# Optimization experiments

Measured on AMD Instinct MI355X. Metric: run time of the kernel, lower is better.

## Reference

```python
import jax, jax.numpy as jnp
import numpy as np
import math

B, D = 4096, 2048  # batch, input_size == hidden_size


def setup_inputs() -> dict:
    key = jax.random.key(0)
    ks = jax.random.split(key, 9)
    stdv = 1.0 / math.sqrt(D)
    u = lambda k, shp: jax.random.uniform(k, shp, jnp.float32, -stdv, stdv)
    return {
        "inputs": jax.random.normal(ks[0], (B, D), jnp.float32),
        "frac_n": jax.random.normal(ks[1], (B, D), jnp.float32),
        "frac_d": jax.random.uniform(ks[2], (B, D), jnp.float32, 0.1, 1.0),
        "scale": jax.random.normal(ks[3], (B, D), jnp.float32),
        "w_r": u(ks[4], (D, D)),
        "w_k": u(ks[5], (D, D)),
        "w_v": u(ks[6], (D, D)),
        "w_o": u(ks[7], (D, D)),
        "w_u": jnp.ones((D,), jnp.float32),  # init.ones_ for 1-D params
        "w_w": jnp.ones((D,), jnp.float32),
    }


def reference(inputs, frac_n, frac_d, scale, w_r, w_k, w_v, w_o, w_u, w_w):
    # r/k/v projections: [B,D] @ [D,D]^T
    r_t = jax.nn.sigmoid(inputs @ w_r.T)
    k_t = inputs @ w_k.T
    v_t = inputs @ w_v.T

    # stabilized WKV update (output path, includes bonus w_u)
    softmax_scale = jnp.maximum(scale, w_u + k_t)
    cell_mult = jnp.exp(scale - softmax_scale)
    attn_mult = jnp.exp(w_u + k_t - softmax_scale)
    frac_n_t = cell_mult * frac_n + attn_mult * v_t
    frac_d_t = cell_mult * frac_d + attn_mult

    # state update path (decay w_w, no bonus)
    next_scale = jnp.maximum(scale + w_w, k_t)
    next_cell_mult = jnp.exp(scale + w_w - next_scale)
    next_attn_mult = jnp.exp(k_t - next_scale)
    next_frac_n = next_cell_mult * frac_n + next_attn_mult * v_t
    next_frac_d = next_cell_mult * frac_d + next_attn_mult

    output = (r_t * (frac_n_t / frac_d_t)) @ w_o.T
    return (output, next_frac_n, next_frac_d, next_scale)
```

## Files before the change

### kernel.cpp

```cpp
#include <hip/hip_runtime.h>
#include <hip/hip_bf16.h>
#include <stdint.h>

#define B_SZ 4096
#define D_SZ 2048

typedef __attribute__((ext_vector_type(4))) float f32x4;
typedef __attribute__((ext_vector_type(8))) __bf16 bf16x8;
typedef __attribute__((ext_vector_type(4))) unsigned short u16x4;
typedef unsigned short u16;

static constexpr long BD = (long)B_SZ * D_SZ;
static constexpr long DD = (long)D_SZ * D_SZ;

__device__ __forceinline__ u16 f2bf(float f) {
  union { float f; unsigned int u; } c; c.f = f;
  unsigned int u = c.u;
  u = (u + 0x7fffu + ((u >> 16) & 1u)) >> 16;
  return (u16)u;
}
__device__ __forceinline__ float bf2f(u16 h) {
  union { unsigned int u; float f; } c; c.u = ((unsigned int)h) << 16;
  return c.f;
}

__global__ __launch_bounds__(256) void k_convert(
    const float* __restrict__ x,  const float* __restrict__ wr,
    const float* __restrict__ wk, const float* __restrict__ wv,
    const float* __restrict__ wo,
    u16* __restrict__ Xb, u16* __restrict__ W3b, u16* __restrict__ Wob) {
  long i = ((long)blockIdx.x * 256 + threadIdx.x) * 4;
  const float* src; u16* dst; long so, dofs;
  if (i < BD)               { src = x;  so = i;            dst = Xb;  dofs = so; }
  else if (i < BD + DD)     { src = wr; so = i - BD;       dst = W3b; dofs = i - BD; }
  else if (i < BD + 2*DD)   { src = wk; so = i - BD - DD;  dst = W3b; dofs = i - BD; }
  else if (i < BD + 3*DD)   { src = wv; so = i - BD - 2*DD; dst = W3b; dofs = i - BD; }
  else                      { src = wo; so = i - BD - 3*DD; dst = Wob; dofs = so; }
  f32x4 v = *reinterpret_cast<const f32x4*>(src + so);
  u16x4 o;
  o[0] = f2bf(v[0]); o[1] = f2bf(v[1]); o[2] = f2bf(v[2]); o[3] = f2bf(v[3]);
  *reinterpret_cast<u16x4*>(dst + dofs) = o;
}

__device__ __forceinline__ void gload16(const u16* g, const u16* l) {
  __builtin_amdgcn_global_load_lds(
      (const __attribute__((address_space(1))) unsigned int*)g,
      (__attribute__((address_space(3))) unsigned int*)l, 16, 0, 0);
}

#define FENCE asm volatile("" ::: "memory")
#define BAR do { FENCE; __builtin_amdgcn_s_barrier(); FENCE; } while (0)
#define VMC(n) asm volatile("s_waitcnt vmcnt(" #n ")" ::: "memory")

template <bool OUT_BF16>
__global__ __launch_bounds__(256, 4) void k_gemm128(
    const u16* __restrict__ A, const u16* __restrict__ Bm,
    void* __restrict__ C, int M, int N, int K) {
  __shared__ __align__(16) u16 lds[32768];
  const int tid = threadIdx.x;
  const int l   = tid & 63;
  const int w   = tid >> 6;
  const int wm  = w >> 1, wn = w & 1;
  const int bm = blockIdx.y, bn = blockIdx.x;
  const int NT = K >> 6;

  const int gcol  = (((l & 7) ^ (l >> 3)) << 3);
  const int grow  = w * 32 + (l >> 3);
  const u16* Abase = A  + (long)(bm * 128 + grow) * K + gcol;
  const u16* Bbase = Bm + (long)(bn * 128 + grow) * K + gcol;
  const int sdst = w * 2048;

  #define STAGE(t) do {                                              \
    const long _ko = (long)(t) * 64;                                 \
    u16* _da = &lds[((t) & 1) * 16384 + sdst];                       \
    u16* _db = _da + 8192;                                           \
    _Pragma("unroll")                                                \
    for (int _c = 0; _c < 4; ++_c) {                                 \
      gload16(Abase + (long)_c * 8 * K + _ko, _da + _c * 512);       \
      gload16(Bbase + (long)_c * 8 * K + _ko, _db + _c * 512);       \
    }                                                                \
  } while (0)

  const int rby  = (l & 15) * 128;
  const int obx0 = ((l >> 4) * 16) ^ ((l & 7) << 4);
  const int lo0  = (rby + obx0) >> 1;
  const int lo1  = lo0 ^ 32;

  f32x4 acc[4][4] = {};

  auto COMPUTE = [&](int p) {
#pragma unroll
    for (int ks = 0; ks < 2; ++ks) {
      const int lo = ks ? lo1 : lo0;
      bf16x8 af[4], bf[4];
#pragma unroll
      for (int mi = 0; mi < 4; ++mi)
        af[mi] = *reinterpret_cast<const bf16x8*>(
            &lds[p * 16384 + (wm * 4 + mi) * 1024 + lo]);
#pragma unroll
      for (int ni = 0; ni < 4; ++ni)
        bf[ni] = *reinterpret_cast<const bf16x8*>(
            &lds[p * 16384 + 8192 + (wn * 4 + ni) * 1024 + lo]);
      __builtin_amdgcn_s_setprio(1);
#pragma unroll
      for (int mi = 0; mi < 4; ++mi)
#pragma unroll
        for (int ni = 0; ni < 4; ++ni)
          acc[mi][ni] = __builtin_amdgcn_mfma_f32_16x16x32_bf16(
              af[mi], bf[ni], acc[mi][ni], 0, 0, 0);
      __builtin_amdgcn_s_setprio(0);
    }
  };

  STAGE(0);
  VMC(0); BAR;

  for (int t = 0; t < NT - 1; ++t) {
    STAGE(t + 1);
    COMPUTE(t & 1);
    VMC(0); BAR;
  }
  COMPUTE((NT - 1) & 1);
  #undef STAGE

  const int rb = (l >> 4) * 4, cb = l & 15;
  const long Crow0 = (long)bm * 128 + wm * 64 + rb;
  const long Ccol0 = (long)bn * 128 + wn * 64 + cb;
#pragma unroll
  for (int mi = 0; mi < 4; ++mi)
#pragma unroll
    for (int ni = 0; ni < 4; ++ni)
#pragma unroll
      for (int r = 0; r < 4; ++r) {
        const long gr = Crow0 + mi * 16 + r;
        const long gc = Ccol0 + ni * 16;
        if constexpr (OUT_BF16)
          ((u16*)C)[gr * N + gc] = f2bf(acc[mi][ni][r]);
        else
          ((float*)C)[gr * N + gc] = acc[mi][ni][r];
      }
}

__global__ __launch_bounds__(256) void k_elem(
    const u16* __restrict__ rkv,
    const float* __restrict__ frac_n, const float* __restrict__ frac_d,
    const float* __restrict__ scale,
    const float* __restrict__ w_u, const float* __restrict__ w_w,
    float* __restrict__ o_nfn, float* __restrict__ o_nfd,
    float* __restrict__ o_ns,  u16* __restrict__ a_b) {
  const long idx4 = ((long)blockIdx.x * 256 + threadIdx.x) * 4;
  const int d = (int)(idx4 % D_SZ);
  const long rbase = (idx4 / D_SZ) * (3 * (long)D_SZ) + d;

  u16x4 r4 = *reinterpret_cast<const u16x4*>(rkv + rbase);
  u16x4 k4 = *reinterpret_cast<const u16x4*>(rkv + rbase + D_SZ);
  u16x4 v4 = *reinterpret_cast<const u16x4*>(rkv + rbase + 2 * D_SZ);
  f32x4 fn = *reinterpret_cast<const f32x4*>(frac_n + idx4);
  f32x4 fd = *reinterpret_cast<const f32x4*>(frac_d + idx4);
  f32x4 sc = *reinterpret_cast<const f32x4*>(scale + idx4);
  f32x4 wu = *reinterpret_cast<const f32x4*>(w_u + d);
  f32x4 ww = *reinterpret_cast<const f32x4*>(w_w + d);

  f32x4 onf, ond, ons; u16x4 oa;
#pragma unroll
  for (int j = 0; j < 4; ++j) {
    const float r = 1.0f / (1.0f + __expf(-bf2f(r4[j])));
    const float k = bf2f(k4[j]);
    const float v = bf2f(v4[j]);
    const float s = sc[j], n = fn[j], dn = fd[j];

    const float ss  = fmaxf(s, wu[j] + k);
    const float cm  = __expf(s - ss);
    const float am  = __expf(wu[j] + k - ss);
    const float fnt = cm * n + am * v;
    const float fdt = cm * dn + am;

    const float ns  = fmaxf(s + ww[j], k);
    const float ncm = __expf(s + ww[j] - ns);
    const float nam = __expf(k - ns);
    onf[j] = ncm * n + nam * v;
    ond[j] = ncm * dn + nam;
    ons[j] = ns;
    oa[j]  = f2bf(r * (fnt / fdt));
  }
  *reinterpret_cast<f32x4*>(o_nfn + idx4) = onf;
  *reinterpret_cast<f32x4*>(o_nfd + idx4) = ond;
  *reinterpret_cast<f32x4*>(o_ns  + idx4) = ons;
  *reinterpret_cast<u16x4*>(a_b   + idx4) = oa;
}

extern "C" void kernel_launch(void* const* d_in, const int* in_sizes, int n_in,
                              void* d_out, int out_size, void* d_ws, size_t ws_size,
                              hipStream_t stream) {
  const float* x      = (const float*)d_in[0];
  const float* frac_n = (const float*)d_in[1];
  const float* frac_d = (const float*)d_in[2];
  const float* scale  = (const float*)d_in[3];
  const float* wr     = (const float*)d_in[4];
  const float* wk     = (const float*)d_in[5];
  const float* wv     = (const float*)d_in[6];
  const float* wo     = (const float*)d_in[7];
  const float* wu     = (const float*)d_in[8];
  const float* ww     = (const float*)d_in[9];
  float* out = (float*)d_out;

  u16* Xb   = (u16*)d_ws;
  u16* W3b  = Xb + BD;
  u16* Wob  = W3b + 3 * DD;
  u16* rkvb = Wob + DD;
  u16* ab   = rkvb + 3 * BD;

  {
    const long total = BD + 4 * DD;
    const int blocks = (int)(total / 4 / 256);
    k_convert<<<blocks, 256, 0, stream>>>(x, wr, wk, wv, wo, Xb, W3b, Wob);
  }
  k_gemm128<true><<<dim3(3 * D_SZ / 128, B_SZ / 128), 256, 0, stream>>>(
      Xb, W3b, rkvb, B_SZ, 3 * D_SZ, D_SZ);
  k_elem<<<(int)(BD / 4 / 256), 256, 0, stream>>>(
      rkvb, frac_n, frac_d, scale, wu, ww,
      out + BD, out + 2 * BD, out + 3 * BD, ab);
  k_gemm128<false><<<dim3(D_SZ / 128, B_SZ / 128), 256, 0, stream>>>(
      ab, Wob, out, B_SZ, D_SZ, D_SZ);
}
```

Measured before the change: 220.6 us.

## Fuse r/k/v projection GEMM with WKV elementwise epilogue

Replaces the combined r/k/v GEMM plus separate elementwise kernel with a single kernel. Each block computes a 128x64 tile of r, k and v at once and applies sigmoid and the WKV update straight from the fp32 accumulators. This removes the bf16 rkv intermediate write and read-back and one kernel launch, and k/v are no longer rounded to bf16 before the update. In exchange the epilogue uses uncoalesced scalar loads and stores, occupancy drops to 2 blocks per CU, and the larger LDS footprint and 24 accumulators per lane raise register pressure.

```diff
diff --git a/kernel.cpp b/kernel.cpp
--- a/kernel.cpp
+++ b/kernel.cpp
@@ -52,6 +52,130 @@
 #define BAR do { FENCE; __builtin_amdgcn_s_barrier(); FENCE; } while (0)
 #define VMC(n) asm volatile("s_waitcnt vmcnt(" #n ")" ::: "memory")
 
+__global__ __launch_bounds__(256, 2) void k_fused(
+    const u16* __restrict__ A, const u16* __restrict__ W3,
+    const float* __restrict__ frac_n, const float* __restrict__ frac_d,
+    const float* __restrict__ scale,
+    const float* __restrict__ w_u, const float* __restrict__ w_w,
+    float* __restrict__ o_nfn, float* __restrict__ o_nfd,
+    float* __restrict__ o_ns,  u16* __restrict__ ab) {
+  __shared__ __align__(16) u16 lds[40960];
+  const int tid = threadIdx.x;
+  const int l   = tid & 63;
+  const int w   = tid >> 6;
+  const int wm  = w >> 1, wn = w & 1;
+  const int bm = blockIdx.y, bn = blockIdx.x;
+  const int K  = D_SZ;
+  const int NT = K >> 6;
+
+  const int gcol = (((l & 7) ^ (l >> 3)) << 3);
+  const u16* Abase = A  + (long)(bm * 128 + w * 32 + (l >> 3)) * K + gcol;
+  const u16* Rbase = W3 +          (long)(bn * 64 + w * 16 + (l >> 3)) * K + gcol;
+  const u16* Kbase = W3 + DD     + (long)(bn * 64 + w * 16 + (l >> 3)) * K + gcol;
+  const u16* Vbase = W3 + 2 * DD + (long)(bn * 64 + w * 16 + (l >> 3)) * K + gcol;
+  const int Asd = w * 2048;
+  const int Bsd = w * 1024;
+
+  #define STAGE(t) do {                                                  \
+    const long _ko = (long)(t) * 64;                                     \
+    u16* _buf = &lds[((t) & 1) * 20480];                                 \
+    _Pragma("unroll")                                                    \
+    for (int _c = 0; _c < 4; ++_c)                                       \
+      gload16(Abase + (long)_c * 8 * K + _ko, _buf + Asd + _c * 512);    \
+    _Pragma("unroll")                                                    \
+    for (int _c = 0; _c < 2; ++_c) {                                     \
+      gload16(Rbase + (long)_c * 8 * K + _ko, _buf +  8192 + Bsd + _c * 512); \
+      gload16(Kbase + (long)_c * 8 * K + _ko, _buf + 12288 + Bsd + _c * 512); \
+      gload16(Vbase + (long)_c * 8 * K + _ko, _buf + 16384 + Bsd + _c * 512); \
+    }                                                                    \
+  } while (0)
+
+  const int rby  = (l & 15) * 128;
+  const int obx0 = ((l >> 4) * 16) ^ ((l & 7) << 4);
+  const int lo0  = (rby + obx0) >> 1;
+  const int lo1  = lo0 ^ 32;
+
+  f32x4 acc[3][4][2] = {};
+
+  auto COMPUTE = [&](int p) {
+    const int base = p * 20480;
+#pragma unroll
+    for (int ks = 0; ks < 2; ++ks) {
+      const int lo = ks ? lo1 : lo0;
+      bf16x8 af[4], fb[3][2];
+#pragma unroll
+      for (int mi = 0; mi < 4; ++mi)
+        af[mi] = *reinterpret_cast<const bf16x8*>(
+            &lds[base + (wm * 4 + mi) * 1024 + lo]);
+#pragma unroll
+      for (int j = 0; j < 3; ++j)
+#pragma unroll
+        for (int ni = 0; ni < 2; ++ni)
+          fb[j][ni] = *reinterpret_cast<const bf16x8*>(
+              &lds[base + 8192 + j * 4096 + (wn * 2 + ni) * 1024 + lo]);
+      __builtin_amdgcn_s_setprio(1);
+#pragma unroll
+      for (int j = 0; j < 3; ++j)
+#pragma unroll
+        for (int mi = 0; mi < 4; ++mi)
+#pragma unroll
+          for (int ni = 0; ni < 2; ++ni)
+            acc[j][mi][ni] = __builtin_amdgcn_mfma_f32_16x16x32_bf16(
+                af[mi], fb[j][ni], acc[j][mi][ni], 0, 0, 0);
+      __builtin_amdgcn_s_setprio(0);
+    }
+  };
+
+  STAGE(0);
+  VMC(0); BAR;
+  for (int t = 0; t < NT - 1; ++t) {
+    STAGE(t + 1);
+    COMPUTE(t & 1);
+    VMC(0); BAR;
+  }
+  COMPUTE((NT - 1) & 1);
+  #undef STAGE
+
+  const int rb = (l >> 4) * 4, cb = l & 15;
+  const long row0 = (long)bm * 128 + wm * 64 + rb;
+  const long col0 = (long)bn * 64 + wn * 32 + cb;
+#pragma unroll
+  for (int mi = 0; mi < 4; ++mi)
+#pragma unroll
+    for (int ni = 0; ni < 2; ++ni) {
+      const long gc  = col0 + ni * 16;
+      const float wuv = w_u[gc];
+      const float wwv = w_w[gc];
+#pragma unroll
+      for (int r = 0; r < 4; ++r) {
+        const long gr  = row0 + mi * 16 + r;
+        const long idx = gr * D_SZ + gc;
+        const float rr = acc[0][mi][ni][r];
+        const float kk = acc[1][mi][ni][r];
+        const float vv = acc[2][mi][ni][r];
+        const float n  = frac_n[idx];
+        const float dn = frac_d[idx];
+        const float s  = scale[idx];
+
+        const float rt  = 1.0f / (1.0f + __expf(-rr));
+        const float ss  = fmaxf(s, wuv + kk);
+        const float cm  = __expf(s - ss);
+        const float am  = __expf(wuv + kk - ss);
+        const float fnt = cm * n + am * vv;
+        const float fdt = cm * dn + am;
+
+        const float ns2 = fmaxf(s + wwv, kk);
+        const float ncm = __expf(s + wwv - ns2);
+        const float nam = __expf(kk - ns2);
+
+        o_nfn[idx] = ncm * n + nam * vv;
+        o_nfd[idx] = ncm * dn + nam;
+        o_ns[idx]  = ns2;
+        ab[idx]    = f2bf(rt * (fnt / fdt));
+      }
+    }
+}
+
 template <bool OUT_BF16>
 __global__ __launch_bounds__(256, 4) void k_gemm128(
     const u16* __restrict__ A, const u16* __restrict__ Bm,
@@ -114,7 +238,6 @@
 
   STAGE(0);
   VMC(0); BAR;
-
   for (int t = 0; t < NT - 1; ++t) {
     STAGE(t + 1);
     COMPUTE(t & 1);
@@ -139,54 +262,6 @@
         else
           ((float*)C)[gr * N + gc] = acc[mi][ni][r];
       }
-}
-
-__global__ __launch_bounds__(256) void k_elem(
-    const u16* __restrict__ rkv,
-    const float* __restrict__ frac_n, const float* __restrict__ frac_d,
-    const float* __restrict__ scale,
-    const float* __restrict__ w_u, const float* __restrict__ w_w,
-    float* __restrict__ o_nfn, float* __restrict__ o_nfd,
-    float* __restrict__ o_ns,  u16* __restrict__ a_b) {
-  const long idx4 = ((long)blockIdx.x * 256 + threadIdx.x) * 4;
-  const int d = (int)(idx4 % D_SZ);
-  const long rbase = (idx4 / D_SZ) * (3 * (long)D_SZ) + d;
-
-  u16x4 r4 = *reinterpret_cast<const u16x4*>(rkv + rbase);
-  u16x4 k4 = *reinterpret_cast<const u16x4*>(rkv + rbase + D_SZ);
-  u16x4 v4 = *reinterpret_cast<const u16x4*>(rkv + rbase + 2 * D_SZ);
-  f32x4 fn = *reinterpret_cast<const f32x4*>(frac_n + idx4);
-  f32x4 fd = *reinterpret_cast<const f32x4*>(frac_d + idx4);
-  f32x4 sc = *reinterpret_cast<const f32x4*>(scale + idx4);
-  f32x4 wu = *reinterpret_cast<const f32x4*>(w_u + d);
-  f32x4 ww = *reinterpret_cast<const f32x4*>(w_w + d);
-
-  f32x4 onf, ond, ons; u16x4 oa;
-#pragma unroll
-  for (int j = 0; j < 4; ++j) {
-    const float r = 1.0f / (1.0f + __expf(-bf2f(r4[j])));
-    const float k = bf2f(k4[j]);
-    const float v = bf2f(v4[j]);
-    const float s = sc[j], n = fn[j], dn = fd[j];
-
-    const float ss  = fmaxf(s, wu[j] + k);
-    const float cm  = __expf(s - ss);
-    const float am  = __expf(wu[j] + k - ss);
-    const float fnt = cm * n + am * v;
-    const float fdt = cm * dn + am;
-
-    const float ns  = fmaxf(s + ww[j], k);
-    const float ncm = __expf(s + ww[j] - ns);
-    const float nam = __expf(k - ns);
-    onf[j] = ncm * n + nam * v;
-    ond[j] = ncm * dn + nam;
-    ons[j] = ns;
-    oa[j]  = f2bf(r * (fnt / fdt));
-  }
-  *reinterpret_cast<f32x4*>(o_nfn + idx4) = onf;
-  *reinterpret_cast<f32x4*>(o_nfd + idx4) = ond;
-  *reinterpret_cast<f32x4*>(o_ns  + idx4) = ons;
-  *reinterpret_cast<u16x4*>(a_b   + idx4) = oa;
 }
 
 extern "C" void kernel_launch(void* const* d_in, const int* in_sizes, int n_in,
@@ -207,18 +282,15 @@
   u16* Xb   = (u16*)d_ws;
   u16* W3b  = Xb + BD;
   u16* Wob  = W3b + 3 * DD;
-  u16* rkvb = Wob + DD;
-  u16* ab   = rkvb + 3 * BD;
+  u16* ab   = Wob + DD;
 
   {
     const long total = BD + 4 * DD;
     const int blocks = (int)(total / 4 / 256);
     k_convert<<<blocks, 256, 0, stream>>>(x, wr, wk, wv, wo, Xb, W3b, Wob);
   }
-  k_gemm128<true><<<dim3(3 * D_SZ / 128, B_SZ / 128), 256, 0, stream>>>(
-      Xb, W3b, rkvb, B_SZ, 3 * D_SZ, D_SZ);
-  k_elem<<<(int)(BD / 4 / 256), 256, 0, stream>>>(
-      rkvb, frac_n, frac_d, scale, wu, ww,
+  k_fused<<<dim3(D_SZ / 64, B_SZ / 128), 256, 0, stream>>>(
+      Xb, W3b, frac_n, frac_d, scale, wu, ww,
       out + BD, out + 2 * BD, out + 3 * BD, ab);
   k_gemm128<false><<<dim3(D_SZ / 128, B_SZ / 128), 256, 0, stream>>>(
       ab, Wob, out, B_SZ, D_SZ, D_SZ);
```

Result: faster. 203.0 us (-8.0%).
